# Performance work log

Measured on AMD Instinct MI355X. Metric: run time of the kernel, lower is better.

## Reference

```python
import math
import jax, jax.numpy as jnp
import numpy as np

NUM_EXPERTS = 4
CAPACITY_FACTOR = 1.0
AUX_W = 0.01
Z_W = 0.001


def setup_inputs() -> dict:
    key = jax.random.key(0)
    k1, k2 = jax.random.split(key)
    B, T, C = 16, 2048, 896
    x = jax.random.normal(k1, (B, T, C), dtype=jnp.float32)
    # nn.Linear(C, E, bias=False) with normal_(std=0.02): weight shape [E, C]
    W = jax.random.normal(k2, (NUM_EXPERTS, C), dtype=jnp.float32) * 0.02
    return {"x": x, "W": W}


def reference(x, W):
    B, T, C = x.shape
    E = W.shape[0]
    N = B * T
    capacity = math.ceil(N * CAPACITY_FACTOR / E)  # static from shapes

    router_logits = jnp.einsum('btc,ec->bte', x, W)          # [B,T,E]
    router_probs = jax.nn.softmax(router_logits, axis=-1)     # [B,T,E]
    expert_indices = jnp.argmax(router_probs, axis=-1)        # [B,T]
    assign = jax.nn.one_hot(expert_indices, E, dtype=jnp.bool_)  # [B,T,E]

    # Per-expert scores: assigned tokens keep their prob, others -> -inf.
    # top_k of size `capacity` per expert; entries with -inf are invalid
    # (i.e. fewer than `capacity` tokens were assigned), matching
    # top-min(num_assigned, capacity) in the torch loop.
    scores = jnp.where(assign, router_probs, -jnp.inf)        # [B,T,E]
    scores_en = scores.reshape(N, E).T                        # [E,N]
    top_vals, top_idx = jax.lax.top_k(scores_en, capacity)    # [E,capacity]
    valid = (top_vals > -jnp.inf).astype(jnp.float32)         # [E,capacity]

    dispatch_flat = jnp.zeros((N, E), jnp.float32)
    # scatter per-expert selections; .max so invalid (0.0) writes are no-ops
    dispatch_flat = dispatch_flat.at[top_idx, jnp.arange(E)[:, None]].max(valid)
    dispatch_mask = dispatch_flat.reshape(B, T, E)
    gates = dispatch_mask

    # Aux load-balancing loss
    f = dispatch_mask.mean(axis=(0, 1))                        # [E]
    P = router_probs.mean(axis=(0, 1))                         # [E]
    aux_loss = AUX_W * (f * P).sum() * E
    # Router z-loss
    z_loss = Z_W * jnp.mean(jnp.square(jax.nn.logsumexp(router_logits, axis=-1)))

    return gates, dispatch_mask, aux_loss + z_loss
```

## Files before the change

kernel.cpp:

```cpp
#include <hip/hip_runtime.h>
#include <stdint.h>

#define N_TOK 32768
#define C_DIM 896
#define C2    448
#define E_NUM 4
#define CAP   8192
#define NBINS 16384
#define BASE_BITS 0x3E800000u


__device__ __forceinline__ int binOf(uint32_t bits) {
    if (bits <= BASE_BITS) return 0;
    uint32_t d = (bits - BASE_BITS) >> 10;
    return d > 16383u ? 16383 : (int)d;
}

__global__ __launch_bounds__(1024) void k_router(const float2* __restrict__ x2,
                                                 const float* __restrict__ Wg,
                                                 uint32_t* __restrict__ hist,
                                                 double* __restrict__ partials,
                                                 float* __restrict__ probf,
                                                 int* __restrict__ expert)
{
    __shared__ float2 wsh[E_NUM * C2];
    __shared__ double red[16][5];
    int tid = threadIdx.x;

    float* wf = (float*)wsh;
    for (int i = tid; i < E_NUM * C_DIM; i += 1024) wf[i] = Wg[i];
    __syncthreads();

    int wave = tid >> 6, lane = tid & 63;
    int t = blockIdx.x * 16 + wave;

    double acc0 = 0, acc1 = 0, acc2 = 0, acc3 = 0;
    const float2* xr = x2 + (size_t)t * C2;
#pragma unroll
    for (int k = 0; k < 7; ++k) {
        int c = lane + 64 * k;
        float2 xv = xr[c];
        double dx = (double)xv.x, dy = (double)xv.y;
        float2 w0 = wsh[0 * C2 + c];
        float2 w1 = wsh[1 * C2 + c];
        float2 w2 = wsh[2 * C2 + c];
        float2 w3 = wsh[3 * C2 + c];
        acc0 += dx * (double)w0.x; acc0 += dy * (double)w0.y;
        acc1 += dx * (double)w1.x; acc1 += dy * (double)w1.y;
        acc2 += dx * (double)w2.x; acc2 += dy * (double)w2.y;
        acc3 += dx * (double)w3.x; acc3 += dy * (double)w3.y;
    }
#pragma unroll
    for (int off = 32; off > 0; off >>= 1) {
        acc0 += __shfl_xor(acc0, off);
        acc1 += __shfl_xor(acc1, off);
        acc2 += __shfl_xor(acc2, off);
        acc3 += __shfl_xor(acc3, off);
    }

    if (lane == 0) {
        double m = fmax(fmax(acc0, acc1), fmax(acc2, acc3));
        double e0 = exp(acc0 - m), e1 = exp(acc1 - m), e2 = exp(acc2 - m), e3 = exp(acc3 - m);
        double s = e0 + e1 + e2 + e3;
        double inv = 1.0 / s;
        int best = 0; double bl = acc0;
        if (acc1 > bl) { best = 1; bl = acc1; }
        if (acc2 > bl) { best = 2; bl = acc2; }
        if (acc3 > bl) { best = 3; bl = acc3; }
        double pb = (best == 0 ? e0 : best == 1 ? e1 : best == 2 ? e2 : e3) * inv;
        float pf = (float)pb;
        probf[t]  = pf;
        expert[t] = best;
        atomicAdd(&hist[best * NBINS + binOf(__float_as_uint(pf))], 1u);
        double lse = m + log(s);
        red[wave][0] = e0 * inv; red[wave][1] = e1 * inv;
        red[wave][2] = e2 * inv; red[wave][3] = e3 * inv;
        red[wave][4] = lse * lse;
    }
    __syncthreads();
    if (tid < 5) {
        double v = 0.0;
        for (int w = 0; w < 16; ++w) v += red[w][tid];
        partials[(size_t)blockIdx.x * 5 + tid] = v;
    }
}

__global__ __launch_bounds__(1024) void k_reduce(const uint32_t* __restrict__ hist,
                                                 const double* __restrict__ partials,
                                                 int4* __restrict__ params,
                                                 float* __restrict__ out_scalar)
{
    __shared__ double dred[1024];
    __shared__ uint32_t s[1024];
    __shared__ double finals[5];
    __shared__ int ne_sh[E_NUM];
    int tid = threadIdx.x;

    for (int c = 0; c < 5; ++c) {
        double v = 0.0;
        for (int r = tid; r < 2048; r += 1024) v += partials[(size_t)r * 5 + c];
        dred[tid] = v; __syncthreads();
        for (int off = 512; off > 0; off >>= 1) {
            if (tid < off) dred[tid] += dred[tid + off];
            __syncthreads();
        }
        if (tid == 0) finals[c] = dred[0];
        __syncthreads();
    }

    for (int e = 0; e < E_NUM; ++e) {
        const uint32_t* h = hist + e * NBINS;
        int lo = tid * 16;
        uint32_t csum = 0;
        for (int b = 0; b < 16; ++b) csum += h[lo + b];
        s[tid] = csum; __syncthreads();
        for (int off = 1; off < 1024; off <<= 1) {
            uint32_t v = (tid + off < 1024) ? s[tid + off] : 0u;
            __syncthreads();
            s[tid] += v;
            __syncthreads();
        }
        uint32_t ne = s[0];
        if (tid == 0) ne_sh[e] = (int)ne;
        if (ne <= (uint32_t)CAP) {
            if (tid == 0) params[e] = make_int4(0, -1, 0, (int)ne);
        } else {
            uint32_t S_i = s[tid];
            uint32_t S_next = (tid < 1023) ? s[tid + 1] : 0u;
            if (S_i > (uint32_t)CAP && S_next <= (uint32_t)CAP) {
                uint32_t above = S_next;
                for (int b = lo + 15; b >= lo; --b) {
                    uint32_t hb = h[b];
                    if (above + hb > (uint32_t)CAP) {
                        params[e] = make_int4(1, b, (int)((uint32_t)CAP - above), (int)ne);
                        break;
                    }
                    above += hb;
                }
            }
        }
        __syncthreads();
    }

    if (tid == 0) {
        double aux = 0.0;
        for (int e = 0; e < E_NUM; ++e) {
            double f = (double)(ne_sh[e] < CAP ? ne_sh[e] : CAP) / (double)N_TOK;
            double P = finals[e] / (double)N_TOK;
            aux += f * P;
        }
        aux *= 0.01 * (double)E_NUM;
        double z = 0.001 * (finals[4] / (double)N_TOK);
        *out_scalar = (float)(aux + z);
    }
}

__global__ void k_gather(const float* __restrict__ probf, const int* __restrict__ expert,
                         const int4* __restrict__ params, uint32_t* __restrict__ candcount,
                         uint2* __restrict__ cand)
{
    int t = blockIdx.x * blockDim.x + threadIdx.x;
    if (t >= N_TOK) return;
    int e = expert[t];
    int4 pr = params[e];
    if (pr.x != 1) return;
    uint32_t bits = __float_as_uint(probf[t]);
    if (binOf(bits) == pr.y) {
        uint32_t pos = atomicAdd(&candcount[e], 1u);
        cand[(size_t)e * N_TOK + pos] = make_uint2(bits, (uint32_t)t);
    }
}

__global__ __launch_bounds__(1024) void k_rank(const int4* __restrict__ params,
                                               const uint32_t* __restrict__ candcount,
                                               const uint2* __restrict__ cand,
                                               uint8_t* __restrict__ sel)
{
    int e = blockIdx.x;
    int4 pr = params[e];
    if (pr.x != 1) return;
    int K = (int)candcount[e];
    int krem = pr.z;
    const uint2* ce = cand + (size_t)e * N_TOK;
    for (int i = threadIdx.x; i < K; i += 1024) {
        uint2 ci = ce[i];
        int rank = 0;
        for (int j = 0; j < K; ++j) {
            uint2 cj = ce[j];
            rank += (int)((cj.x > ci.x) || (cj.x == ci.x && cj.y < ci.y));
        }
        sel[ci.y] = (rank < krem) ? (uint8_t)1 : (uint8_t)0;
    }
}

__global__ void k_write(const float* __restrict__ probf, const int* __restrict__ expert,
                        const int4* __restrict__ params, const uint8_t* __restrict__ sel,
                        float4* __restrict__ out)
{
    int t = blockIdx.x * blockDim.x + threadIdx.x;
    if (t >= N_TOK) return;
    int e = expert[t];
    int4 pr = params[e];
    float v;
    if (pr.x == 0) {
        v = 1.0f;
    } else {
        int b = binOf(__float_as_uint(probf[t]));
        v = (b > pr.y) ? 1.0f : (b < pr.y ? 0.0f : (sel[t] ? 1.0f : 0.0f));
    }
    float4 o = make_float4(0.f, 0.f, 0.f, 0.f);
    (&o.x)[e] = v;
    out[t] = o;
    out[t + N_TOK] = o;
}

extern "C" void kernel_launch(void* const* d_in, const int* in_sizes, int n_in,
                              void* d_out, int out_size, void* d_ws, size_t ws_size,
                              hipStream_t stream)
{
    const float* x = (const float*)d_in[0];
    const float* W = (const float*)d_in[1];
    float* out = (float*)d_out;
    char* ws = (char*)d_ws;

    uint32_t* hist      = (uint32_t*)(ws);
    uint32_t* candcount = (uint32_t*)(ws + 262144);
    double*   partials  = (double*)  (ws + 262160);
    float*    probf     = (float*)   (ws + 344080);
    int*      expert    = (int*)     (ws + 475152);
    int4*     params    = (int4*)    (ws + 606224);
    uint2*    cand      = (uint2*)   (ws + 606288);
    uint8_t*  sel       = (uint8_t*) (ws + 1654864);

    hipMemsetAsync(ws, 0, 262160, stream);

    k_router<<<2048, 1024, 0, stream>>>((const float2*)x, W, hist, partials, probf, expert);
    k_reduce<<<1, 1024, 0, stream>>>(hist, partials, params, out + 262144);
    k_gather<<<N_TOK / 256, 256, 0, stream>>>(probf, expert, params, candcount, cand);
    k_rank<<<E_NUM, 1024, 0, stream>>>(params, candcount, cand, sel);
    k_write<<<N_TOK / 256, 256, 0, stream>>>(probf, expert, params, sel, (float4*)out);
}
```

Measured before the change: 219.2 us.

## Fuse gather and output write, scatter rank results directly; use wave shuffles in reduce

The gather and final write kernels are merged into one pass. It writes the dispatch masks immediately, setting boundary-bin tokens to zero, and the rank kernel then sets selected boundary tokens to one directly in the output. This removes one launch, the sel buffer and a re-read of probf/expert. The single-block reduce kernel now uses wave shuffles instead of shared-memory tree reductions and scans, cutting many __syncthreads.

```diff
diff --git a/kernel.cpp b/kernel.cpp
--- a/kernel.cpp
+++ b/kernel.cpp
@@ -90,53 +90,75 @@
                                                  int4* __restrict__ params,
                                                  float* __restrict__ out_scalar)
 {
-    __shared__ double dred[1024];
-    __shared__ uint32_t s[1024];
+    __shared__ double wred[16][5];
     __shared__ double finals[5];
+    __shared__ uint32_t wtot[16], woff[16];
     __shared__ int ne_sh[E_NUM];
-    int tid = threadIdx.x;
-
-    for (int c = 0; c < 5; ++c) {
+    int tid = threadIdx.x, lane = tid & 63, wave = tid >> 6;
+
+    double a0 = 0, a1 = 0, a2 = 0, a3 = 0, a4 = 0;
+    for (int r = tid; r < 2048; r += 1024) {
+        const double* p = partials + (size_t)r * 5;
+        a0 += p[0]; a1 += p[1]; a2 += p[2]; a3 += p[3]; a4 += p[4];
+    }
+#pragma unroll
+    for (int off = 32; off > 0; off >>= 1) {
+        a0 += __shfl_xor(a0, off); a1 += __shfl_xor(a1, off);
+        a2 += __shfl_xor(a2, off); a3 += __shfl_xor(a3, off);
+        a4 += __shfl_xor(a4, off);
+    }
+    if (lane == 0) {
+        wred[wave][0] = a0; wred[wave][1] = a1; wred[wave][2] = a2;
+        wred[wave][3] = a3; wred[wave][4] = a4;
+    }
+    __syncthreads();
+    if (tid < 5) {
         double v = 0.0;
-        for (int r = tid; r < 2048; r += 1024) v += partials[(size_t)r * 5 + c];
-        dred[tid] = v; __syncthreads();
-        for (int off = 512; off > 0; off >>= 1) {
-            if (tid < off) dred[tid] += dred[tid + off];
-            __syncthreads();
-        }
-        if (tid == 0) finals[c] = dred[0];
-        __syncthreads();
+        for (int w = 0; w < 16; ++w) v += wred[w][tid];
+        finals[tid] = v;
     }
 
     for (int e = 0; e < E_NUM; ++e) {
         const uint32_t* h = hist + e * NBINS;
         int lo = tid * 16;
         uint32_t csum = 0;
+#pragma unroll
         for (int b = 0; b < 16; ++b) csum += h[lo + b];
-        s[tid] = csum; __syncthreads();
-        for (int off = 1; off < 1024; off <<= 1) {
-            uint32_t v = (tid + off < 1024) ? s[tid + off] : 0u;
-            __syncthreads();
-            s[tid] += v;
-            __syncthreads();
-        }
-        uint32_t ne = s[0];
-        if (tid == 0) ne_sh[e] = (int)ne;
+
+        uint32_t v = csum;
+#pragma unroll
+        for (int off = 1; off < 64; off <<= 1) {
+            uint32_t u = __shfl_down(v, off);
+            if (lane + off < 64) v += u;
+        }
+        if (lane == 0) wtot[wave] = v;
+        __syncthreads();
+        if (tid < 16) {
+            uint32_t tv = wtot[tid];
+            uint32_t iv = tv;
+#pragma unroll
+            for (int off = 1; off < 16; off <<= 1) {
+                uint32_t u = __shfl_down(iv, off);
+                if (tid + off < 16) iv += u;
+            }
+            woff[tid] = iv - tv;
+            if (tid == 0) ne_sh[e] = (int)iv;
+        }
+        __syncthreads();
+
+        uint32_t S = v + woff[wave];
+        uint32_t ne = (uint32_t)ne_sh[e];
         if (ne <= (uint32_t)CAP) {
             if (tid == 0) params[e] = make_int4(0, -1, 0, (int)ne);
-        } else {
-            uint32_t S_i = s[tid];
-            uint32_t S_next = (tid < 1023) ? s[tid + 1] : 0u;
-            if (S_i > (uint32_t)CAP && S_next <= (uint32_t)CAP) {
-                uint32_t above = S_next;
-                for (int b = lo + 15; b >= lo; --b) {
-                    uint32_t hb = h[b];
-                    if (above + hb > (uint32_t)CAP) {
-                        params[e] = make_int4(1, b, (int)((uint32_t)CAP - above), (int)ne);
-                        break;
-                    }
-                    above += hb;
+        } else if (S > (uint32_t)CAP && S - csum <= (uint32_t)CAP) {
+            uint32_t above = S - csum;
+            for (int b = lo + 15; b >= lo; --b) {
+                uint32_t hb = h[b];
+                if (above + hb > (uint32_t)CAP) {
+                    params[e] = make_int4(1, b, (int)((uint32_t)CAP - above), (int)ne);
+                    break;
                 }
+                above += hb;
             }
         }
         __syncthreads();
@@ -155,26 +177,38 @@
     }
 }
 
-__global__ void k_gather(const float* __restrict__ probf, const int* __restrict__ expert,
-                         const int4* __restrict__ params, uint32_t* __restrict__ candcount,
-                         uint2* __restrict__ cand)
+__global__ void k_gather_write(const float* __restrict__ probf, const int* __restrict__ expert,
+                               const int4* __restrict__ params, uint32_t* __restrict__ candcount,
+                               uint2* __restrict__ cand, float4* __restrict__ out)
 {
     int t = blockIdx.x * blockDim.x + threadIdx.x;
     if (t >= N_TOK) return;
     int e = expert[t];
     int4 pr = params[e];
-    if (pr.x != 1) return;
     uint32_t bits = __float_as_uint(probf[t]);
-    if (binOf(bits) == pr.y) {
-        uint32_t pos = atomicAdd(&candcount[e], 1u);
-        cand[(size_t)e * N_TOK + pos] = make_uint2(bits, (uint32_t)t);
-    }
+    float v;
+    if (pr.x == 0) {
+        v = 1.0f;
+    } else {
+        int b = binOf(bits);
+        if (b == pr.y) {
+            uint32_t pos = atomicAdd(&candcount[e], 1u);
+            cand[(size_t)e * N_TOK + pos] = make_uint2(bits, (uint32_t)t);
+            v = 0.0f;
+        } else {
+            v = (b > pr.y) ? 1.0f : 0.0f;
+        }
+    }
+    float4 o = make_float4(0.f, 0.f, 0.f, 0.f);
+    (&o.x)[e] = v;
+    out[t] = o;
+    out[t + N_TOK] = o;
 }
 
 __global__ __launch_bounds__(1024) void k_rank(const int4* __restrict__ params,
                                                const uint32_t* __restrict__ candcount,
                                                const uint2* __restrict__ cand,
-                                               uint8_t* __restrict__ sel)
+                                               float* __restrict__ outf)
 {
     int e = blockIdx.x;
     int4 pr = params[e];
@@ -189,29 +223,11 @@
             uint2 cj = ce[j];
             rank += (int)((cj.x > ci.x) || (cj.x == ci.x && cj.y < ci.y));
         }
-        sel[ci.y] = (rank < krem) ? (uint8_t)1 : (uint8_t)0;
-    }
-}
-
-__global__ void k_write(const float* __restrict__ probf, const int* __restrict__ expert,
-                        const int4* __restrict__ params, const uint8_t* __restrict__ sel,
-                        float4* __restrict__ out)
-{
-    int t = blockIdx.x * blockDim.x + threadIdx.x;
-    if (t >= N_TOK) return;
-    int e = expert[t];
-    int4 pr = params[e];
-    float v;
-    if (pr.x == 0) {
-        v = 1.0f;
-    } else {
-        int b = binOf(__float_as_uint(probf[t]));
-        v = (b > pr.y) ? 1.0f : (b < pr.y ? 0.0f : (sel[t] ? 1.0f : 0.0f));
-    }
-    float4 o = make_float4(0.f, 0.f, 0.f, 0.f);
-    (&o.x)[e] = v;
-    out[t] = o;
-    out[t + N_TOK] = o;
+        if (rank < krem) {
+            outf[(size_t)ci.y * 4 + e] = 1.0f;
+            outf[((size_t)ci.y + N_TOK) * 4 + e] = 1.0f;
+        }
+    }
 }
 
 extern "C" void kernel_launch(void* const* d_in, const int* in_sizes, int n_in,
@@ -230,13 +246,11 @@
     int*      expert    = (int*)     (ws + 475152);
     int4*     params    = (int4*)    (ws + 606224);
     uint2*    cand      = (uint2*)   (ws + 606288);
-    uint8_t*  sel       = (uint8_t*) (ws + 1654864);
 
     hipMemsetAsync(ws, 0, 262160, stream);
 
     k_router<<<2048, 1024, 0, stream>>>((const float2*)x, W, hist, partials, probf, expert);
     k_reduce<<<1, 1024, 0, stream>>>(hist, partials, params, out + 262144);
-    k_gather<<<N_TOK / 256, 256, 0, stream>>>(probf, expert, params, candcount, cand);
-    k_rank<<<E_NUM, 1024, 0, stream>>>(params, candcount, cand, sel);
-    k_write<<<N_TOK / 256, 256, 0, stream>>>(probf, expert, params, sel, (float4*)out);
-}
+    k_gather_write<<<N_TOK / 256, 256, 0, stream>>>(probf, expert, params, candcount, cand, (float4*)out);
+    k_rank<<<E_NUM, 1024, 0, stream>>>(params, candcount, cand, out);
+}
```

New measurement: 200.0 us. 1.1x faster.
